# Kernel tuning notes

Measured on AMD Instinct MI355X. Metric: run time of the kernel, lower is better.

The kernel has to match this reference:

```python
import jax, jax.numpy as jnp
import numpy as np

BITS = 4
SPLIT_BITS = 4  # `ratio` arg plays the role of split_bits in the torch Function


def _chunk_quant(src, bits):
    """src: [n_chunks, chunk_elems...]; quantize each chunk with its own min/max."""
    reduce_axes = tuple(range(1, src.ndim))
    mn = src.min(axis=reduce_axes, keepdims=True)
    mx = src.max(axis=reduce_axes, keepdims=True)
    levels = jnp.asarray(2 ** bits - 1, src.dtype)
    step = (mx - mn) / levels
    safe_step = jnp.where(step == 0, jnp.ones_like(step), step)
    # torch: round((s-min)/step) - 2^(b-1); then (+2^(b-1))*step + min  ==  round(...)*step + min
    q = jnp.round((src - mn) / safe_step) * safe_step + mn
    # if min == max the chunk is passed through unchanged
    return jnp.where(mn == mx, src, q)


def setup_inputs() -> dict:
    key = jax.random.key(0)
    x = jax.random.normal(key, (16, 2048, 2048), dtype=jnp.float32)
    return {"x": x}


def reference(x) -> jnp.ndarray:
    shape = x.shape
    flat = x.reshape(-1)
    n_chunks = 2 ** SPLIT_BITS  # 16; flat.size divisible by 16 by construction
    order = jnp.argsort(flat)            # ascending sort permutation
    src = flat[order].reshape(n_chunks, -1)
    q = _chunk_quant(src, BITS).reshape(-1)
    # scatter quantized values back to original positions: out[order[i]] = q[i]
    inv = jnp.argsort(order)
    out = q[inv]
    return out.reshape(shape)
```

## Files before the change

kernel.cpp:

```cpp
#include <hip/hip_runtime.h>
#include <math.h>

#define L1B 4096
#define L2B 512
#define L3B 2048
#define SLOTS 32
#define H1_BLOCKS 512
#define H2_BLOCKS 256
#define H2_WORDS (SLOTS * L2B / 2)

__device__ unsigned int g_part1[H1_BLOCKS * L1B];
__device__ unsigned int g_part2[H2_BLOCKS * H2_WORDS];
__device__ unsigned int g_hist1[L1B];
__device__ unsigned int g_hist2[SLOTS * L2B];
__device__ unsigned int g_hist3[SLOTS * L3B];
__device__ unsigned char g_sid1[L1B];
__device__ unsigned char g_sid2[SLOTS * L2B];

__device__ unsigned int g_bin1[32], g_res1[32];
__device__ int          g_slot1[32];
__device__ unsigned int g_bin2[32], g_res2[32];
__device__ int          g_slot2[32];
__device__ unsigned int g_bin3[32], g_res3[32];
__device__ float        g_mn[16], g_mx[16];
__device__ unsigned int g_tkey[16];

__device__ __forceinline__ unsigned int f2key(float f) {
    unsigned int b = __float_as_uint(f);
    return (b & 0x80000000u) ? ~b : (b | 0x80000000u);
}
__device__ __forceinline__ float key2f(unsigned int k) {
    unsigned int b = (k & 0x80000000u) ? (k & 0x7FFFFFFFu) : ~k;
    return __uint_as_float(b);
}

__global__ void zero_scratch() {
    int i = blockIdx.x * blockDim.x + threadIdx.x;
    int stride = gridDim.x * blockDim.x;
    for (int j = i; j < SLOTS * L3B; j += stride) g_hist3[j] = 0u;
    unsigned int* s1 = (unsigned int*)g_sid1;
    for (int j = i; j < L1B / 4; j += stride) s1[j] = 0u;
    unsigned int* s2 = (unsigned int*)g_sid2;
    for (int j = i; j < SLOTS * L2B / 4; j += stride) s2[j] = 0u;
}

__global__ void hist1_kernel(const float4* __restrict__ x, int n4) {
    __shared__ unsigned int h[2 * L1B];
    for (int j = threadIdx.x; j < 2 * L1B; j += blockDim.x) h[j] = 0u;
    __syncthreads();
    unsigned int* hp = &h[((threadIdx.x >> 6) & 1) * L1B];
    int stride = gridDim.x * blockDim.x;
    for (int i = blockIdx.x * blockDim.x + threadIdx.x; i < n4; i += stride) {
        float4 v = x[i];
        atomicAdd(&hp[f2key(v.x) >> 20], 1u);
        atomicAdd(&hp[f2key(v.y) >> 20], 1u);
        atomicAdd(&hp[f2key(v.z) >> 20], 1u);
        atomicAdd(&hp[f2key(v.w) >> 20], 1u);
    }
    __syncthreads();
    for (int j = threadIdx.x; j < L1B; j += blockDim.x)
        g_part1[blockIdx.x * L1B + j] = h[j] + h[L1B + j];
}

__global__ void reduce1_kernel() {
    int j = blockIdx.x * blockDim.x + threadIdx.x;
    if (j >= L1B) return;
    unsigned int s = 0;
    for (int b = 0; b < H1_BLOCKS; ++b) s += g_part1[b * L1B + j];
    g_hist1[j] = s;
}

__device__ void wave_select(const unsigned int* __restrict__ hist, int nbins,
                            unsigned int r, unsigned int* out_bin, unsigned int* out_res) {
    int lane = threadIdx.x & 63;
    unsigned int base = 0;
    for (int k = 0; k < nbins; k += 64) {
        unsigned int v = hist[k + lane];
        unsigned int incl = v;
#pragma unroll
        for (int off = 1; off < 64; off <<= 1) {
            unsigned int t = (unsigned int)__shfl_up((int)incl, off, 64);
            if (lane >= off) incl += t;
        }
        unsigned int total = (unsigned int)__shfl((int)incl, 63, 64);
        if (r < base + total) {
            unsigned long long m = __ballot(base + incl > r);
            int fl = __ffsll((long long)m) - 1;
            unsigned int incl_fl = (unsigned int)__shfl((int)incl, fl, 64);
            unsigned int v_fl = (unsigned int)__shfl((int)v, fl, 64);
            if (lane == 0) {
                *out_bin = (unsigned int)(k + fl);
                *out_res = r - (base + incl_fl - v_fl);
            }
            return;
        }
        base += total;
    }
}

__global__ void select1_kernel(unsigned int n) {
    int i = blockIdx.x;
    unsigned int M = n >> 4;
    unsigned int c = (unsigned int)(i >> 1);
    unsigned int r = (i & 1) ? ((c + 1) * M - 1u) : (c * M);
    wave_select(g_hist1, L1B, r, &g_bin1[i], &g_res1[i]);
}

__global__ void assign1_kernel() {
    if (threadIdx.x != 0 || blockIdx.x != 0) return;
    int nslot = 0;
    for (int i = 0; i < 32; ++i) {
        unsigned int b = g_bin1[i];
        if (g_sid1[b] == 0) g_sid1[b] = (unsigned char)(++nslot);
        g_slot1[i] = g_sid1[b] - 1;
    }
}

__global__ void hist2_kernel(const float4* __restrict__ x, int n4) {
    __shared__ unsigned int h2[H2_WORDS];
    __shared__ unsigned char sid1[L1B];
    for (int j = threadIdx.x; j < H2_WORDS; j += blockDim.x) h2[j] = 0u;
    unsigned int* s1w = (unsigned int*)sid1;
    for (int j = threadIdx.x; j < L1B / 4; j += blockDim.x) s1w[j] = ((const unsigned int*)g_sid1)[j];
    __syncthreads();
    int stride = gridDim.x * blockDim.x;
    for (int i = blockIdx.x * blockDim.x + threadIdx.x; i < n4; i += stride) {
        float4 v = x[i];
        float vv[4] = {v.x, v.y, v.z, v.w};
#pragma unroll
        for (int k = 0; k < 4; ++k) {
            unsigned int key = f2key(vv[k]);
            unsigned int s = sid1[key >> 20];
            if (s) {
                unsigned int c = ((s - 1) << 9) | ((key >> 11) & (L2B - 1));
                atomicAdd(&h2[c >> 1], 1u << ((c & 1) << 4));
            }
        }
    }
    __syncthreads();
    for (int j = threadIdx.x; j < H2_WORDS; j += blockDim.x)
        g_part2[blockIdx.x * H2_WORDS + j] = h2[j];
}

__global__ void reduce2_kernel() {
    int w = blockIdx.x * blockDim.x + threadIdx.x;
    if (w >= H2_WORDS) return;
    unsigned int lo = 0, hi = 0;
    for (int b = 0; b < H2_BLOCKS; ++b) {
        unsigned int u = g_part2[b * H2_WORDS + w];
        lo += u & 0xFFFFu;
        hi += u >> 16;
    }
    g_hist2[2 * w] = lo;
    g_hist2[2 * w + 1] = hi;
}

__global__ void select2_kernel() {
    int i = blockIdx.x;
    int s = g_slot1[i];
    wave_select(g_hist2 + s * L2B, L2B, g_res1[i], &g_bin2[i], &g_res2[i]);
}

__global__ void assign2_kernel() {
    if (threadIdx.x != 0 || blockIdx.x != 0) return;
    int nslot = 0;
    for (int i = 0; i < 32; ++i) {
        int p = g_slot1[i] * L2B + (int)g_bin2[i];
        if (g_sid2[p] == 0) g_sid2[p] = (unsigned char)(++nslot);
        g_slot2[i] = g_sid2[p] - 1;
    }
}

__global__ void hist3_kernel(const float4* __restrict__ x, int n4) {
    __shared__ unsigned char sid1[L1B];
    __shared__ unsigned char sid2[SLOTS * L2B];
    unsigned int* s1w = (unsigned int*)sid1;
    for (int j = threadIdx.x; j < L1B / 4; j += blockDim.x) s1w[j] = ((const unsigned int*)g_sid1)[j];
    unsigned int* s2w = (unsigned int*)sid2;
    for (int j = threadIdx.x; j < SLOTS * L2B / 4; j += blockDim.x) s2w[j] = ((const unsigned int*)g_sid2)[j];
    __syncthreads();
    int stride = gridDim.x * blockDim.x;
    for (int i = blockIdx.x * blockDim.x + threadIdx.x; i < n4; i += stride) {
        float4 v = x[i];
        float vv[4] = {v.x, v.y, v.z, v.w};
#pragma unroll
        for (int k = 0; k < 4; ++k) {
            unsigned int key = f2key(vv[k]);
            unsigned int s = sid1[key >> 20];
            if (s) {
                unsigned int s2 = sid2[((s - 1) << 9) | ((key >> 11) & (L2B - 1))];
                if (s2) atomicAdd(&g_hist3[((s2 - 1) << 11) | (key & (L3B - 1))], 1u);
            }
        }
    }
}

__global__ void select3_kernel() {
    int i = blockIdx.x;
    int s2 = g_slot2[i];
    wave_select(g_hist3 + s2 * L3B, L3B, g_res2[i], &g_bin3[i], &g_res3[i]);
}

__global__ void finalize_kernel() {
    int c = threadIdx.x;
    if (c < 16) {
        unsigned int klo = (g_bin1[2 * c] << 20) | (g_bin2[2 * c] << 11) | g_bin3[2 * c];
        unsigned int khi = (g_bin1[2 * c + 1] << 20) | (g_bin2[2 * c + 1] << 11) | g_bin3[2 * c + 1];
        g_mn[c] = key2f(klo);
        g_mx[c] = key2f(khi);
        g_tkey[c] = (c == 0) ? 0u : klo;
    }
}

__global__ void quant_kernel(const float4* __restrict__ x, float4* __restrict__ out, int n4) {
    __shared__ float s_mn[16], s_mx[16];
    __shared__ unsigned int s_t[16];
    if (threadIdx.x < 16) {
        s_mn[threadIdx.x] = g_mn[threadIdx.x];
        s_mx[threadIdx.x] = g_mx[threadIdx.x];
        s_t[threadIdx.x]  = g_tkey[threadIdx.x];
    }
    __syncthreads();
    int stride = gridDim.x * blockDim.x;
    for (int i = blockIdx.x * blockDim.x + threadIdx.x; i < n4; i += stride) {
        float4 v = x[i];
        float r[4] = {v.x, v.y, v.z, v.w};
#pragma unroll
        for (int k = 0; k < 4; ++k) {
            float xv = r[k];
            unsigned int key = f2key(xv);
            int c = (key >= s_t[8]) ? 8 : 0;
            if (key >= s_t[c + 4]) c += 4;
            if (key >= s_t[c + 2]) c += 2;
            if (key >= s_t[c + 1]) c += 1;
            float mn = s_mn[c], mx = s_mx[c];
            float outv;
            if (mn == mx) {
                outv = xv;
            } else {
                float st = (mx - mn) / 15.0f;
                if (st == 0.0f) st = 1.0f;
                float q = rintf((xv - mn) / st);
                outv = __fadd_rn(__fmul_rn(q, st), mn);
            }
            r[k] = outv;
        }
        out[i] = make_float4(r[0], r[1], r[2], r[3]);
    }
}

extern "C" void kernel_launch(void* const* d_in, const int* in_sizes, int n_in,
                              void* d_out, int out_size, void* d_ws, size_t ws_size,
                              hipStream_t stream) {
    const float* x = (const float*)d_in[0];
    float* out = (float*)d_out;
    int n  = in_sizes[0];
    int n4 = n / 4;

    zero_scratch<<<128, 256, 0, stream>>>();
    hist1_kernel<<<H1_BLOCKS, 512, 0, stream>>>((const float4*)x, n4);
    reduce1_kernel<<<16, 256, 0, stream>>>();
    select1_kernel<<<32, 64, 0, stream>>>((unsigned int)n);
    assign1_kernel<<<1, 64, 0, stream>>>();
    hist2_kernel<<<H2_BLOCKS, 512, 0, stream>>>((const float4*)x, n4);
    reduce2_kernel<<<32, 256, 0, stream>>>();
    select2_kernel<<<32, 64, 0, stream>>>();
    assign2_kernel<<<1, 64, 0, stream>>>();
    hist3_kernel<<<2048, 256, 0, stream>>>((const float4*)x, n4);
    select3_kernel<<<32, 64, 0, stream>>>();
    finalize_kernel<<<1, 64, 0, stream>>>();
    quant_kernel<<<4096, 256, 0, stream>>>((const float4*)x, (float4*)out, n4);
}
```

Before: 742.6 us.

## Replace three-pass radix select with two-pass 14/18-bit histogram selection

Cuts the radix-select from three histogram passes (12/9/11 bits) to two (14/18 bits), removing one full read of the input. The first pass uses 16-bit packed shared counters; the second pass writes atomics straight to a global 2^18-bin per-slot histogram, and a coarse 256-group summary keeps selection to two-level wave scans. Slot assignment is folded into the select kernel and several small launches are merged, lowering launch overhead. In exchange it adds global atomic contention in hist2, a larger zeroing pass (32×2^18 words), and risks 16-bit overflow in per-block counters if a block sees more than 65535 keys in one bin.

Measured after the change: 921.3 us. 24.1% more time.

```diff
diff --git a/kernel.cpp b/kernel.cpp
--- a/kernel.cpp
+++ b/kernel.cpp
@@ -1,27 +1,24 @@
 #include <hip/hip_runtime.h>
 #include <math.h>
 
-#define L1B 4096
-#define L2B 512
-#define L3B 2048
+#define L1B 16384
+#define L1W (L1B / 2)
+#define H1_BLOCKS 512
 #define SLOTS 32
-#define H1_BLOCKS 512
-#define H2_BLOCKS 256
-#define H2_WORDS (SLOTS * L2B / 2)
-
-__device__ unsigned int g_part1[H1_BLOCKS * L1B];
-__device__ unsigned int g_part2[H2_BLOCKS * H2_WORDS];
+#define L2BITS 18
+#define L2B (1 << L2BITS)
+#define L2GROUPS (L2B / 256)
+
+__device__ unsigned int g_part1[H1_BLOCKS * L1W];
 __device__ unsigned int g_hist1[L1B];
+__device__ unsigned int g_coarse1[L1B / 256];
 __device__ unsigned int g_hist2[SLOTS * L2B];
-__device__ unsigned int g_hist3[SLOTS * L3B];
+__device__ unsigned int g_coarse2[SLOTS * L2GROUPS];
 __device__ unsigned char g_sid1[L1B];
-__device__ unsigned char g_sid2[SLOTS * L2B];
+__device__ int          g_nslot;
 
 __device__ unsigned int g_bin1[32], g_res1[32];
 __device__ int          g_slot1[32];
-__device__ unsigned int g_bin2[32], g_res2[32];
-__device__ int          g_slot2[32];
-__device__ unsigned int g_bin3[32], g_res3[32];
 __device__ float        g_mn[16], g_mx[16];
 __device__ unsigned int g_tkey[16];
 
@@ -37,41 +34,50 @@
 __global__ void zero_scratch() {
     int i = blockIdx.x * blockDim.x + threadIdx.x;
     int stride = gridDim.x * blockDim.x;
-    for (int j = i; j < SLOTS * L3B; j += stride) g_hist3[j] = 0u;
+    for (int j = i; j < SLOTS * L2B; j += stride) g_hist2[j] = 0u;
+    for (int j = i; j < L1B; j += stride) g_hist1[j] = 0u;
     unsigned int* s1 = (unsigned int*)g_sid1;
     for (int j = i; j < L1B / 4; j += stride) s1[j] = 0u;
-    unsigned int* s2 = (unsigned int*)g_sid2;
-    for (int j = i; j < SLOTS * L2B / 4; j += stride) s2[j] = 0u;
+    if (i < L1B / 256) g_coarse1[i] = 0u;
 }
 
 __global__ void hist1_kernel(const float4* __restrict__ x, int n4) {
-    __shared__ unsigned int h[2 * L1B];
-    for (int j = threadIdx.x; j < 2 * L1B; j += blockDim.x) h[j] = 0u;
-    __syncthreads();
-    unsigned int* hp = &h[((threadIdx.x >> 6) & 1) * L1B];
+    __shared__ unsigned int h[L1W];
+    for (int j = threadIdx.x; j < L1W; j += blockDim.x) h[j] = 0u;
+    __syncthreads();
     int stride = gridDim.x * blockDim.x;
     for (int i = blockIdx.x * blockDim.x + threadIdx.x; i < n4; i += stride) {
         float4 v = x[i];
-        atomicAdd(&hp[f2key(v.x) >> 20], 1u);
-        atomicAdd(&hp[f2key(v.y) >> 20], 1u);
-        atomicAdd(&hp[f2key(v.z) >> 20], 1u);
-        atomicAdd(&hp[f2key(v.w) >> 20], 1u);
-    }
-    __syncthreads();
-    for (int j = threadIdx.x; j < L1B; j += blockDim.x)
-        g_part1[blockIdx.x * L1B + j] = h[j] + h[L1B + j];
+        float vv[4] = {v.x, v.y, v.z, v.w};
+#pragma unroll
+        for (int k = 0; k < 4; ++k) {
+            unsigned int b = f2key(vv[k]) >> L2BITS;
+            atomicAdd(&h[b >> 1], 1u << ((b & 1) << 4));
+        }
+    }
+    __syncthreads();
+    for (int j = threadIdx.x; j < L1W; j += blockDim.x)
+        g_part1[blockIdx.x * L1W + j] = h[j];
 }
 
 __global__ void reduce1_kernel() {
-    int j = blockIdx.x * blockDim.x + threadIdx.x;
-    if (j >= L1B) return;
-    unsigned int s = 0;
-    for (int b = 0; b < H1_BLOCKS; ++b) s += g_part1[b * L1B + j];
-    g_hist1[j] = s;
-}
-
-__device__ void wave_select(const unsigned int* __restrict__ hist, int nbins,
-                            unsigned int r, unsigned int* out_bin, unsigned int* out_res) {
+    int t = blockIdx.x * blockDim.x + threadIdx.x;
+    int w = t & (L1W - 1);
+    int chunk = t >> 13;
+    unsigned int lo = 0, hi = 0;
+    for (int b = chunk * 64; b < chunk * 64 + 64; ++b) {
+        unsigned int u = g_part1[b * L1W + w];
+        lo += u & 0xFFFFu;
+        hi += u >> 16;
+    }
+    atomicAdd(&g_hist1[2 * w], lo);
+    atomicAdd(&g_hist1[2 * w + 1], hi);
+    atomicAdd(&g_coarse1[w >> 7], lo + hi);
+}
+
+__device__ __forceinline__ void wave_select(const unsigned int* __restrict__ hist,
+                                            int nbins, unsigned int r,
+                                            unsigned int* out_bin, unsigned int* out_res) {
     int lane = threadIdx.x & 63;
     unsigned int base = 0;
     for (int k = 0; k < nbins; k += 64) {
@@ -88,38 +94,47 @@
             int fl = __ffsll((long long)m) - 1;
             unsigned int incl_fl = (unsigned int)__shfl((int)incl, fl, 64);
             unsigned int v_fl = (unsigned int)__shfl((int)v, fl, 64);
-            if (lane == 0) {
-                *out_bin = (unsigned int)(k + fl);
-                *out_res = r - (base + incl_fl - v_fl);
-            }
+            *out_bin = (unsigned int)(k + fl);
+            *out_res = r - (base + incl_fl - v_fl);
             return;
         }
         base += total;
     }
+    *out_bin = (unsigned int)(nbins - 1);
+    *out_res = 0;
 }
 
 __global__ void select1_kernel(unsigned int n) {
-    int i = blockIdx.x;
+    __shared__ unsigned int s_bin[32], s_res[32];
+    int wid = threadIdx.x >> 6;
     unsigned int M = n >> 4;
-    unsigned int c = (unsigned int)(i >> 1);
-    unsigned int r = (i & 1) ? ((c + 1) * M - 1u) : (c * M);
-    wave_select(g_hist1, L1B, r, &g_bin1[i], &g_res1[i]);
-}
-
-__global__ void assign1_kernel() {
-    if (threadIdx.x != 0 || blockIdx.x != 0) return;
-    int nslot = 0;
-    for (int i = 0; i < 32; ++i) {
-        unsigned int b = g_bin1[i];
-        if (g_sid1[b] == 0) g_sid1[b] = (unsigned char)(++nslot);
-        g_slot1[i] = g_sid1[b] - 1;
+    for (int i = wid; i < 32; i += 16) {
+        unsigned int c = (unsigned int)(i >> 1);
+        unsigned int r = (i & 1) ? ((c + 1) * M - 1u) : (c * M);
+        unsigned int g, rg, b, res;
+        wave_select(g_coarse1, L1B / 256, r, &g, &rg);
+        wave_select(g_hist1 + (g << 8), 256, rg, &b, &res);
+        if ((threadIdx.x & 63) == 0) { s_bin[i] = (g << 8) | b; s_res[i] = res; }
+    }
+    __syncthreads();
+    if (threadIdx.x == 0) {
+        unsigned int uniq[32];
+        int nu = 0;
+        for (int i = 0; i < 32; ++i) {
+            unsigned int b = s_bin[i];
+            int s = -1;
+            for (int j = 0; j < nu; ++j) if (uniq[j] == b) { s = j; break; }
+            if (s < 0) { s = nu; uniq[nu++] = b; g_sid1[b] = (unsigned char)(s + 1); }
+            g_slot1[i] = s;
+            g_bin1[i] = b;
+            g_res1[i] = s_res[i];
+        }
+        g_nslot = nu;
     }
 }
 
 __global__ void hist2_kernel(const float4* __restrict__ x, int n4) {
-    __shared__ unsigned int h2[H2_WORDS];
     __shared__ unsigned char sid1[L1B];
-    for (int j = threadIdx.x; j < H2_WORDS; j += blockDim.x) h2[j] = 0u;
     unsigned int* s1w = (unsigned int*)sid1;
     for (int j = threadIdx.x; j < L1B / 4; j += blockDim.x) s1w[j] = ((const unsigned int*)g_sid1)[j];
     __syncthreads();
@@ -130,82 +145,42 @@
 #pragma unroll
         for (int k = 0; k < 4; ++k) {
             unsigned int key = f2key(vv[k]);
-            unsigned int s = sid1[key >> 20];
-            if (s) {
-                unsigned int c = ((s - 1) << 9) | ((key >> 11) & (L2B - 1));
-                atomicAdd(&h2[c >> 1], 1u << ((c & 1) << 4));
-            }
-        }
-    }
-    __syncthreads();
-    for (int j = threadIdx.x; j < H2_WORDS; j += blockDim.x)
-        g_part2[blockIdx.x * H2_WORDS + j] = h2[j];
-}
-
-__global__ void reduce2_kernel() {
-    int w = blockIdx.x * blockDim.x + threadIdx.x;
-    if (w >= H2_WORDS) return;
-    unsigned int lo = 0, hi = 0;
-    for (int b = 0; b < H2_BLOCKS; ++b) {
-        unsigned int u = g_part2[b * H2_WORDS + w];
-        lo += u & 0xFFFFu;
-        hi += u >> 16;
-    }
-    g_hist2[2 * w] = lo;
-    g_hist2[2 * w + 1] = hi;
+            unsigned int s = sid1[key >> L2BITS];
+            if (s) atomicAdd(&g_hist2[((s - 1) << L2BITS) | (key & (L2B - 1))], 1u);
+        }
+    }
+}
+
+__global__ void coarse2_kernel() {
+    int gw = (blockIdx.x * blockDim.x + threadIdx.x) >> 6;
+    int slot = gw >> 10;
+    if (slot >= g_nslot) return;
+    int lane = threadIdx.x & 63;
+    const uint4* p = (const uint4*)&g_hist2[gw << 8];
+    uint4 v = p[lane];
+    unsigned int s = v.x + v.y + v.z + v.w;
+#pragma unroll
+    for (int off = 32; off; off >>= 1) s += (unsigned int)__shfl_down((int)s, off, 64);
+    if (lane == 0) g_coarse2[gw] = s;
 }
 
 __global__ void select2_kernel() {
-    int i = blockIdx.x;
-    int s = g_slot1[i];
-    wave_select(g_hist2 + s * L2B, L2B, g_res1[i], &g_bin2[i], &g_res2[i]);
-}
-
-__global__ void assign2_kernel() {
-    if (threadIdx.x != 0 || blockIdx.x != 0) return;
-    int nslot = 0;
-    for (int i = 0; i < 32; ++i) {
-        int p = g_slot1[i] * L2B + (int)g_bin2[i];
-        if (g_sid2[p] == 0) g_sid2[p] = (unsigned char)(++nslot);
-        g_slot2[i] = g_sid2[p] - 1;
-    }
-}
-
-__global__ void hist3_kernel(const float4* __restrict__ x, int n4) {
-    __shared__ unsigned char sid1[L1B];
-    __shared__ unsigned char sid2[SLOTS * L2B];
-    unsigned int* s1w = (unsigned int*)sid1;
-    for (int j = threadIdx.x; j < L1B / 4; j += blockDim.x) s1w[j] = ((const unsigned int*)g_sid1)[j];
-    unsigned int* s2w = (unsigned int*)sid2;
-    for (int j = threadIdx.x; j < SLOTS * L2B / 4; j += blockDim.x) s2w[j] = ((const unsigned int*)g_sid2)[j];
-    __syncthreads();
-    int stride = gridDim.x * blockDim.x;
-    for (int i = blockIdx.x * blockDim.x + threadIdx.x; i < n4; i += stride) {
-        float4 v = x[i];
-        float vv[4] = {v.x, v.y, v.z, v.w};
-#pragma unroll
-        for (int k = 0; k < 4; ++k) {
-            unsigned int key = f2key(vv[k]);
-            unsigned int s = sid1[key >> 20];
-            if (s) {
-                unsigned int s2 = sid2[((s - 1) << 9) | ((key >> 11) & (L2B - 1))];
-                if (s2) atomicAdd(&g_hist3[((s2 - 1) << 11) | (key & (L3B - 1))], 1u);
-            }
-        }
-    }
-}
-
-__global__ void select3_kernel() {
-    int i = blockIdx.x;
-    int s2 = g_slot2[i];
-    wave_select(g_hist3 + s2 * L3B, L3B, g_res2[i], &g_bin3[i], &g_res3[i]);
-}
-
-__global__ void finalize_kernel() {
-    int c = threadIdx.x;
-    if (c < 16) {
-        unsigned int klo = (g_bin1[2 * c] << 20) | (g_bin2[2 * c] << 11) | g_bin3[2 * c];
-        unsigned int khi = (g_bin1[2 * c + 1] << 20) | (g_bin2[2 * c + 1] << 11) | g_bin3[2 * c + 1];
+    __shared__ unsigned int s_key[32];
+    int wid = threadIdx.x >> 6;
+    for (int i = wid; i < 32; i += 16) {
+        int s = g_slot1[i];
+        unsigned int r = g_res1[i];
+        unsigned int g, rg, b, res;
+        wave_select(g_coarse2 + (s << 10), L2GROUPS, r, &g, &rg);
+        wave_select(g_hist2 + (s << L2BITS) + (g << 8), 256, rg, &b, &res);
+        if ((threadIdx.x & 63) == 0)
+            s_key[i] = (g_bin1[i] << L2BITS) | (g << 8) | b;
+    }
+    __syncthreads();
+    if (threadIdx.x < 16) {
+        int c = threadIdx.x;
+        unsigned int klo = s_key[2 * c];
+        unsigned int khi = s_key[2 * c + 1];
         g_mn[c] = key2f(klo);
         g_mx[c] = key2f(khi);
         g_tkey[c] = (c == 0) ? 0u : klo;
@@ -257,17 +232,12 @@
     int n  = in_sizes[0];
     int n4 = n / 4;
 
-    zero_scratch<<<128, 256, 0, stream>>>();
+    zero_scratch<<<2048, 256, 0, stream>>>();
     hist1_kernel<<<H1_BLOCKS, 512, 0, stream>>>((const float4*)x, n4);
-    reduce1_kernel<<<16, 256, 0, stream>>>();
-    select1_kernel<<<32, 64, 0, stream>>>((unsigned int)n);
-    assign1_kernel<<<1, 64, 0, stream>>>();
-    hist2_kernel<<<H2_BLOCKS, 512, 0, stream>>>((const float4*)x, n4);
-    reduce2_kernel<<<32, 256, 0, stream>>>();
-    select2_kernel<<<32, 64, 0, stream>>>();
-    assign2_kernel<<<1, 64, 0, stream>>>();
-    hist3_kernel<<<2048, 256, 0, stream>>>((const float4*)x, n4);
-    select3_kernel<<<32, 64, 0, stream>>>();
-    finalize_kernel<<<1, 64, 0, stream>>>();
+    reduce1_kernel<<<256, 256, 0, stream>>>();
+    select1_kernel<<<1, 1024, 0, stream>>>((unsigned int)n);
+    hist2_kernel<<<512, 512, 0, stream>>>((const float4*)x, n4);
+    coarse2_kernel<<<8192, 256, 0, stream>>>();
+    select2_kernel<<<1, 1024, 0, stream>>>();
     quant_kernel<<<4096, 256, 0, stream>>>((const float4*)x, (float4*)out, n4);
 }
```
